# Kernel optimization log

Measured on AMD Instinct MI355X. Metric: run time of the kernel, lower is better.

## Reference

```python
import jax, jax.numpy as jnp
import numpy as np

GROUP = 16   # self.group
K = 3        # self.k (top-3 motif rows)


def _unfold3(x):
    # nn.Unfold(kernel_size=3): [B,C,H,W] -> [B, C*9, (H-2)*(W-2)]
    # torch channel ordering: c-major, then kernel offsets row-major.
    B, C, H, W = x.shape
    Ho, Wo = H - 2, W - 2
    pats = jnp.stack([x[:, :, i:i + Ho, j:j + Wo]
                      for i in range(3) for j in range(3)], axis=2)  # [B,C,9,Ho,Wo]
    return pats.reshape(B, C * 9, Ho * Wo)


def _fold3(y, H, W):
    # nn.Fold(output_size=(H,W), kernel_size=3): sum overlapping patches back.
    B, C9, L = y.shape
    C = C9 // 9
    Ho, Wo = H - 2, W - 2
    y = y.reshape(B, C, 3, 3, Ho, Wo)
    out = jnp.zeros((B, C, H, W), y.dtype)
    for i in range(3):
        for j in range(3):
            out = out.at[:, :, i:i + Ho, j:j + Wo].add(y[:, :, i, j])
    return out


def _group_motif(xg, H, W):
    motif = _unfold3(xg)                                  # [B,P,L], P = Cg*9
    B, P, L = motif.shape
    # torch.cdist (p=2) between the P rows, via the Gram trick.
    sq = jnp.sum(motif * motif, axis=-1)                  # [B,P]
    gram = jnp.einsum('bpl,bql->bpq', motif, motif)       # [B,P,P]
    d2 = sq[:, :, None] + sq[:, None, :] - 2.0 * gram
    dist = jnp.sqrt(jnp.maximum(d2, 0.0))
    eye = jnp.eye(P, dtype=bool)[None]
    dist = jnp.where(eye, jnp.inf, dist)                  # diagonal := inf
    # topk(k=1, largest=False) == argmin over last dim
    min_idx = jnp.argmin(dist, axis=-1)                   # [B,P] int
    # torch.unique(return_counts=True) over the whole tensor (flattened over batch)
    counts = jnp.bincount(min_idx.ravel(), length=P)      # [P] int
    # sort counts descending, take first K uniques -> lax.top_k
    top_c, top_i = jax.lax.top_k(counts, K)               # [K],[K]
    total = jnp.sum(top_c).astype(motif.dtype)
    rows = motif[:, top_i, :]                             # [B,K,L] gathered motif rows
    cf = top_c.astype(motif.dtype)
    motif_new = jnp.zeros_like(motif)
    for o in range(K):
        # torch: motif * motif[:, u_o].unsqueeze(1) * c_o // total  (floor division)
        motif_new = motif_new + jnp.floor(motif * rows[:, o][:, None, :] * cf[o] / total)
    return _fold3(motif_new, H, W)


def setup_inputs() -> dict:
    key = jax.random.key(0)
    feature = jax.random.normal(key, (2, 256, 192, 192), dtype=jnp.float32)
    return {"feature": feature}


def reference(feature):
    B, C, H, W = feature.shape
    chunks = jnp.split(feature, GROUP, axis=1)
    outs = [_group_motif(g, H, W) for g in chunks]
    return jnp.concatenate(outs, axis=1)                  # [B, C, H, W]
```

## Files before the change

### kernel.cpp

```cpp
#include <hip/hip_runtime.h>
#include <math.h>

#define NB 2
#define NC 256
#define CG 16
#define HH 192
#define WW 192
#define HO 190
#define PP 144

typedef float v2f __attribute__((ext_vector_type(2)));

#define SMEM_FLOATS 5684

#define GLD16(GP, LP)                                                         \
    __builtin_amdgcn_global_load_lds(                                         \
        (const __attribute__((address_space(1))) void*)(GP),                  \
        (__attribute__((address_space(3))) void*)(LP), 16, 0, 0)

__global__ __launch_bounds__(192, 2) void gram_kernel(const float* __restrict__ x,
                                                      double* __restrict__ gram)
{
    __shared__ __align__(16) float smem[SMEM_FLOATS];
    float* const red2 = smem + 2548;
    float* const ebuf = smem + 4948;

    const int v = threadIdx.x;
    const int p = v & 1;
    const int bb = (v + 2) & ~1;

    const int bid = blockIdx.x;
    const int vx = bid & 7;
    const int tq = bid >> 3;
    const int idxw = tq / 36;
    const int rr0 = tq - idxw * 36;
    const int hg = idxw * 8 + vx;
    const int bg = hg >> 1;
    int r = rr0 + 36 * (hg & 1);
    int c2 = 0;
    while (r >= (c2 + 2) / 2) { r -= (c2 + 2) / 2; ++c2; }
    const int c1a = 2 * r;
    int c1b = 2 * r + 1;
    const bool bval = (c1b <= c2);
    if (!bval) c1b = c2;
    const int b = bg >> 4, g = bg & 15;

    const float* __restrict__ xa  = x + ((size_t)(b * NC + g * CG + c1a)) * (HH * WW);
    const float* __restrict__ xb  = x + ((size_t)(b * NC + g * CG + c1b)) * (HH * WW);
    const float* __restrict__ x2g = x + ((size_t)(b * NC + g * CG + c2 )) * (HH * WW);

    v2f midA[15], midB[15];
#pragma unroll
    for (int o = 0; o < 15; ++o) { midA[o] = (v2f){0.f, 0.f}; midB[o] = (v2f){0.f, 0.f}; }

    v2f win[6][3];
    float ca[6], cb[6];
#pragma unroll
    for (int k = 0; k < 6; ++k) {
        ca[k] = xa[(size_t)(2 + k) * WW + v];
        cb[k] = xb[(size_t)(2 + k) * WW + v];
    }

    const float* pa = xa + (size_t)8 * WW + v;
    const float* pb = xb + (size_t)8 * WW + v;
    int lds_off;

#define USTEP6(P, WPF, GPF)                                                   \
    {                                                                         \
        const float a1 = ca[(P)];                                             \
        const float b1 = cb[(P)];                                             \
        if (GPF) { ca[(P)] = pa[(P) * WW]; cb[(P)] = pb[(P) * WW]; }          \
        if (WPF) {                                                            \
            _Pragma("unroll")                                                 \
            for (int pr = 0; pr < 3; ++pr)                                    \
                win[((P) + 5) % 6][pr] = *(const v2f*)(&smem[lds_off + 2 * pr]); \
        }                                                                     \
        lds_off += 196;                                                       \
        const v2f a2 = (v2f){a1, a1};                                         \
        const v2f b2 = (v2f){b1, b1};                                         \
        _Pragma("unroll")                                                     \
        for (int kk = 0; kk < 5; ++kk) {                                      \
            _Pragma("unroll")                                                 \
            for (int pr = 0; pr < 3; ++pr) {                                  \
                const v2f wv = win[((P) + kk) % 6][pr];                       \
                midA[kk * 3 + pr] = __builtin_elementwise_fma(a2, wv, midA[kk * 3 + pr]); \
                midB[kk * 3 + pr] = __builtin_elementwise_fma(b2, wv, midB[kk * 3 + pr]); \
            }                                                                 \
        }                                                                     \
    }

#define STAGE(ROW0, NROUND, LASTN)                                            \
    __syncthreads();                                                          \
    _Pragma("unroll")                                                         \
    for (int rr2 = 0; rr2 < (NROUND); ++rr2) {                                \
        if (rr2 < (NROUND) - 1 || v < (LASTN)) {                              \
            const int slot = rr2 * 192 + v;                                   \
            const int row = slot / 49;                                        \
            const int s49 = slot - row * 49;                                  \
            const int col = (s49 == 0) ? 0 : (s49 - 1) * 4;                   \
            const float* gp2 = x2g + (size_t)((ROW0) + row) * WW + col;       \
            float* lp = smem + (rr2 * 192 + (v & ~63)) * 4;                   \
            GLD16(gp2, lp);                                                   \
        }                                                                     \
    }                                                                         \
    __syncthreads();                                                          \
    if (v < 116) smem[(v >> 2) * 196 + (v & 3)] = 0.f;                        \
    __syncthreads();

    for (int band = 0; band < 7; ++band) {
        STAGE(band * 24, 8, 77)

        if (band == 0) {
#pragma unroll
            for (int k = 0; k < 5; ++k)
#pragma unroll
            for (int pr = 0; pr < 3; ++pr)
                win[k][pr] = *(const v2f*)(&smem[k * 196 + bb + 2 * pr]);
        }

        lds_off = 5 * 196 + bb;
        for (int it = 0; it < 4; ++it) {
            USTEP6(0, 1, 1) USTEP6(1, 1, 1) USTEP6(2, 1, 1)
            USTEP6(3, 1, 1) USTEP6(4, 1, 1) USTEP6(5, 1, 1)
            pa += 6 * WW; pb += 6 * WW;
        }
    }
    STAGE(168, 7, 24)
    lds_off = 5 * 196 + bb;
    USTEP6(0, 1, 1) USTEP6(1, 1, 1) USTEP6(2, 1, 1)
    USTEP6(3, 1, 1) USTEP6(4, 1, 1) USTEP6(5, 1, 1)
    pa += 6 * WW; pb += 6 * WW;
    USTEP6(0, 1, 1) USTEP6(1, 1, 1) USTEP6(2, 1, 1)
    USTEP6(3, 1, 1) USTEP6(4, 1, 1) USTEP6(5, 1, 1)
    pa += 6 * WW; pb += 6 * WW;
    USTEP6(0, 1, 1) USTEP6(1, 1, 1) USTEP6(2, 1, 0)
    USTEP6(3, 1, 0) USTEP6(4, 1, 0) USTEP6(5, 1, 0)
    USTEP6(0, 1, 0) USTEP6(1, 0, 0)
#undef USTEP6
#undef STAGE

    __syncthreads();
    for (int i = 0; i < 12; ++i) {
        const int ar = (i < 6) ? (i - 2) : (188 + i - 6);
        const float val = (ar >= 0 && ar <= 191) ? x2g[(size_t)ar * WW + v] : 0.f;
        smem[i * 196 + 4 + v] = val;
    }
    __syncthreads();

    double* const gp = gram + (size_t)bg * (PP * PP);

#define EPI_CW(KQ, DJ, CVAL)                                                  \
    ({                                                                        \
        float ve_, vo_;                                                       \
        { const int pr_ = (DJ) >> 1, ln_ = (DJ) & 1;                          \
          const v2f m_ = ((CVAL) == 0) ? midA[(KQ) * 3 + pr_] : midB[(KQ) * 3 + pr_]; \
          ve_ = ln_ ? m_.y : m_.x; }                                          \
        { const int pr_ = ((DJ) + 1) >> 1, ln_ = ((DJ) + 1) & 1;              \
          const v2f m_ = ((CVAL) == 0) ? midA[(KQ) * 3 + pr_] : midB[(KQ) * 3 + pr_]; \
          vo_ = ln_ ? m_.y : m_.x; }                                          \
        float cw_ = p ? vo_ : ve_;                                            \
        cw_ = fmaf(xra, smem[bufa * 196 + 2 + v + (DJ)], cw_);                \
        cw_ = fmaf(xrb, smem[bufb * 196 + 2 + v + (DJ)], cw_);                \
        cw_;                                                                  \
    })

#pragma unroll
    for (int i1 = 0; i1 < 3; ++i1) {
        const int ra = (i1 == 0) ? 0 : ((i1 == 1) ? 1 : 190);
        const int rb = (i1 == 0) ? 1 : ((i1 == 1) ? 190 : 191);
#pragma unroll
        for (int c = 0; c < 2; ++c) {
            const float* __restrict__ xc = (c == 0) ? xa : xb;
            const float xra = xc[(size_t)ra * WW + v];
            const float xrb = xc[(size_t)rb * WW + v];
            if (v >= 96) {
#pragma unroll
                for (int k = 0; k < 5; ++k) {
                    const int bufa = (ra < 2) ? (ra + k) : (ra + k - 184);
                    const int bufb = (rb < 2) ? (rb + k) : (rb + k - 184);
#pragma unroll
                    for (int dj = 0; dj < 5; ++dj)
                        red2[(v - 96) * 25 + k * 5 + dj] = EPI_CW(k, dj, c);
                }
            } else if (v < 2) {
#pragma unroll
                for (int k = 0; k < 5; ++k) {
                    const int bufa = (ra < 2) ? (ra + k) : (ra + k - 184);
                    const int bufb = (rb < 2) ? (rb + k) : (rb + k - 184);
#pragma unroll
                    for (int dj = 0; dj < 5; ++dj)
                        ebuf[v * 25 + k * 5 + dj] = EPI_CW(k, dj, c);
                }
            }
            __syncthreads();
            float e0 = 0.f, e1 = 0.f, e190 = 0.f, e191 = 0.f;
            if (v < 25) {
                e0   = ebuf[v];
                e1   = ebuf[25 + v];
                e190 = red2[94 * 25 + v];
                e191 = red2[95 * 25 + v];
            }
            __syncthreads();
            if (v < 96) {
#pragma unroll
                for (int k = 0; k < 5; ++k) {
                    const int bufa = (ra < 2) ? (ra + k) : (ra + k - 184);
                    const int bufb = (rb < 2) ? (rb + k) : (rb + k - 184);
#pragma unroll
                    for (int dj = 0; dj < 5; ++dj)
                        red2[v * 25 + k * 5 + dj] += EPI_CW(k, dj, c);
                }
            }
            __syncthreads();
#pragma unroll
            for (int s = 48; s >= 3; s >>= 1) {
                for (int idx = v; idx < s * 25; idx += 192) {
                    const int vv = idx / 25, o = idx - vv * 25;
                    red2[vv * 25 + o] += red2[(vv + s) * 25 + o];
                }
                __syncthreads();
            }
            if (v < 25 && (c == 0 || bval)) {
                const int di = v / 5 - 2, dj = v - (v / 5) * 5 - 2;
                const int i2 = i1 + di;
                if (i2 >= 0 && i2 <= 2) {
                    const float S = red2[0 * 25 + v] + red2[1 * 25 + v] + red2[2 * 25 + v];
                    const int c1 = (c == 0) ? c1a : c1b;
#pragma unroll
                    for (int j1 = 0; j1 < 3; ++j1) {
                        const int j2 = j1 + dj;
                        if (j2 < 0 || j2 > 2) continue;
                        const float W = S - ((j1 == 0) ? (e190 + e191)
                                          : (j1 == 1) ? (e0 + e191)
                                                      : (e0 + e1));
                        const int pp = c1 * 9 + i1 * 3 + j1;
                        const int qq = c2 * 9 + i2 * 3 + j2;
                        gp[pp * PP + qq] = (double)W;
                        if (c1 != c2) gp[qq * PP + pp] = (double)W;
                    }
                }
            }
            __syncthreads();
        }
    }
#undef EPI_CW
}

__global__ __launch_bounds__(320) void topk_kernel(const double* __restrict__ gram,
                                                   float* __restrict__ pf,
                                                   int* __restrict__ pi)
{
    const int g = blockIdx.x;
    __shared__ double sdiag[2][PP];
    __shared__ int counts[PP];
    const int tid = threadIdx.x;
    if (tid < PP) counts[tid] = 0;
    if (tid < 2 * PP) {
        const int b = tid / PP, p = tid % PP;
        const double* gb = gram + (size_t)(b * 16 + g) * (PP * PP);
        sdiag[b][p] = gb[p * PP + p];
    }
    __syncthreads();
    if (tid < 2 * PP) {
        const int b = tid / PP, p = tid % PP;
        const double* row = gram + ((size_t)(b * 16 + g) * PP + p) * PP;
        const double sp = sdiag[b][p];
        double best = 1e300;
        int bi = 0;
        for (int q = 0; q < PP; ++q) {
            if (q == p) continue;
            const double d2 = sp + sdiag[b][q] - 2.0 * row[q];
            if (d2 < best) { best = d2; bi = q; }
        }
        atomicAdd(&counts[bi], 1);
    }
    __syncthreads();
    if (tid == 0) {
        int sel[3], cv[3];
        for (int o = 0; o < 3; ++o) {
            int bc = -1, bp = 0;
            for (int p = 0; p < PP; ++p) {
                bool taken = false;
                for (int u = 0; u < o; ++u) if (sel[u] == p) taken = true;
                if (!taken && counts[p] > bc) { bc = counts[p]; bp = p; }
            }
            sel[o] = bp; cv[o] = bc;
        }
        const int tot = cv[0] + cv[1] + cv[2];
        for (int o = 0; o < 3; ++o) {
            pf[g * 4 + o] = (float)cv[o];
            pi[g * 4 + o] = sel[o];
        }
        pf[g * 4 + 3] = (float)tot;
    }
}

template <bool EDGE>
__device__ __forceinline__ void motif_quad(const float* __restrict__ x,
                                           const float* __restrict__ pf,
                                           const int* __restrict__ pi,
                                           float* __restrict__ out,
                                           int b, int ch, int h, int w0)
{
    const int g = ch >> 4;
    const size_t base = ((size_t)(b * NC + ch)) * (HH * WW);
    const float4 xv4 = *(const float4*)(x + base + (size_t)h * WW + w0);
    const float xs[4] = {xv4.x, xv4.y, xv4.z, xv4.w};
    float acc[4] = {0.f, 0.f, 0.f, 0.f};
    const float total = pf[g * 4 + 3];
    const float rcp = (float)(1.0 / (double)total);

#pragma unroll
    for (int o = 0; o < 3; ++o) {
        const int p = pi[g * 4 + o];
        const float cff = pf[g * 4 + o];
        const int co = p / 9;
        const int kk = p - co * 9;
        const int io = kk / 3, jo = kk - (kk / 3) * 3;
        const float* Rb = x + ((size_t)(b * NC + g * CG + co)) * (HH * WW);
#pragma unroll
        for (int i = 0; i < 3; ++i) {
            const int ho = h - i;
            bool rowok = true;
            int hr = ho + io;
            if (EDGE) {
                rowok = (ho >= 0) && (ho < HO);
                hr = hr < 0 ? 0 : (hr > HH - 1 ? HH - 1 : hr);
            }
            const float* row = Rb + (size_t)hr * WW;
            float rv[6];
#pragma unroll
            for (int u = 0; u < 6; ++u) {
                int col = w0 - 2 + jo + u;
                if (EDGE) col = col < 0 ? 0 : (col > WW - 1 ? WW - 1 : col);
                rv[u] = row[col];
            }
#pragma unroll
            for (int j = 0; j < 3; ++j)
#pragma unroll
            for (int q = 0; q < 4; ++q) {
                const float r2 = rv[q - j + 2];
                const float t1 = xs[q] * r2;
                const float t2 = t1 * cff;
                const float q0 = t2 * rcp;
                const float rr = fmaf(-total, q0, t2);
                const float qf = fmaf(rr, rcp, q0);
                const float vfl = floorf(qf);
                if (EDGE) {
                    const int wo = w0 + q - j;
                    const bool ok = rowok && (wo >= 0) && (wo < HO);
                    acc[q] += ok ? vfl : 0.f;
                } else {
                    acc[q] += vfl;
                }
            }
        }
    }
    float4 ov = make_float4(acc[0], acc[1], acc[2], acc[3]);
    *(float4*)(out + base + (size_t)h * WW + w0) = ov;
}

#define NBLK_INT 17296
#define NBLK_EDGE 1136

__global__ __launch_bounds__(256) void out_kernel(const float* __restrict__ x,
                                                  const float* __restrict__ pf,
                                                  const int* __restrict__ pi,
                                                  float* __restrict__ out)
{
    const int bid = blockIdx.x;
    if (bid < NBLK_INT) {
        const int gid = bid * 256 + threadIdx.x;
        const int w4i = gid % 46;
        int t = gid / 46;
        const int h = 2 + t % 188; t /= 188;
        const int ch = t & 255;
        const int b = t >> 8;
        motif_quad<false>(x, pf, pi, out, b, ch, h, (w4i + 1) * 4);
    } else {
        const int gid = (bid - NBLK_INT) * 256 + threadIdx.x;
        const int e = gid % 568;
        int t = gid / 568;
        const int ch = t & 255;
        const int b = t >> 8;
        int h, w4;
        if (e < 192) {
            const int hs = e / 48;
            h = (hs < 2) ? hs : 188 + hs;
            w4 = e % 48;
        } else {
            const int e2 = e - 192;
            h = 2 + (e2 >> 1);
            w4 = (e2 & 1) ? 47 : 0;
        }
        motif_quad<true>(x, pf, pi, out, b, ch, h, w4 * 4);
    }
}

extern "C" void kernel_launch(void* const* d_in, const int* in_sizes, int n_in,
                              void* d_out, int out_size, void* d_ws, size_t ws_size,
                              hipStream_t stream)
{
    const float* x = (const float*)d_in[0];
    float* out = (float*)d_out;

    double* gram = (double*)d_ws;
    const size_t gram_bytes = (size_t)32 * PP * PP * sizeof(double);
    float* pf = (float*)((char*)d_ws + gram_bytes);
    int* pi = (int*)((char*)d_ws + gram_bytes + 256);

    gram_kernel<<<2304, 192, 0, stream>>>(x, gram);
    topk_kernel<<<16, 320, 0, stream>>>(gram, pf, pi);
    out_kernel<<<NBLK_INT + NBLK_EDGE, 256, 0, stream>>>(x, pf, pi, out);
}
```

Measured before the change: 351.2 us.

## Merge two-channel epilogue reduction, hoist LDS pad zeroing, pack interior motif math

The gram kernel epilogue now reduces both channel columns (c1a and c1b) in a single pass, using a 51-float stride, which halves the number of barrier-separated reduction rounds. The zeroing of the LDS pad columns moves out of every band stage to one write before the loop, and pad-column global loads are skipped, which removes one barrier per band. The interior output kernel uses packed v2f multiplies and FMAs for the floor-division math. The trade-off is more LDS per block, which can reduce occupancy, and extra register pressure in the epilogue.

```diff
diff --git a/kernel.cpp b/kernel.cpp
--- a/kernel.cpp
+++ b/kernel.cpp
@@ -11,7 +11,7 @@
 
 typedef float v2f __attribute__((ext_vector_type(2)));
 
-#define SMEM_FLOATS 5684
+#define SMEM_FLOATS 7544
 
 #define GLD16(GP, LP)                                                         \
     __builtin_amdgcn_global_load_lds(                                         \
@@ -23,7 +23,7 @@
 {
     __shared__ __align__(16) float smem[SMEM_FLOATS];
     float* const red2 = smem + 2548;
-    float* const ebuf = smem + 4948;
+    float* const ebuf = smem + 7444;
 
     const int v = threadIdx.x;
     const int p = v & 1;
@@ -48,6 +48,9 @@
     const float* __restrict__ xa  = x + ((size_t)(b * NC + g * CG + c1a)) * (HH * WW);
     const float* __restrict__ xb  = x + ((size_t)(b * NC + g * CG + c1b)) * (HH * WW);
     const float* __restrict__ x2g = x + ((size_t)(b * NC + g * CG + c2 )) * (HH * WW);
+
+    if (v < 116) smem[(v >> 2) * 196 + (v & 3)] = 0.f;
+    else if (v < 118) smem[5568 + v] = 0.f;
 
     v2f midA[15], midB[15];
 #pragma unroll
@@ -97,14 +100,13 @@
             const int slot = rr2 * 192 + v;                                   \
             const int row = slot / 49;                                        \
             const int s49 = slot - row * 49;                                  \
-            const int col = (s49 == 0) ? 0 : (s49 - 1) * 4;                   \
-            const float* gp2 = x2g + (size_t)((ROW0) + row) * WW + col;       \
-            float* lp = smem + (rr2 * 192 + (v & ~63)) * 4;                   \
-            GLD16(gp2, lp);                                                   \
+            if (s49 != 0) {                                                   \
+                const float* gp2 = x2g + (size_t)((ROW0) + row) * WW + (s49 - 1) * 4; \
+                float* lp = smem + (rr2 * 192 + (v & ~63)) * 4;               \
+                GLD16(gp2, lp);                                               \
+            }                                                                 \
         }                                                                     \
     }                                                                         \
-    __syncthreads();                                                          \
-    if (v < 116) smem[(v >> 2) * 196 + (v & 3)] = 0.f;                        \
     __syncthreads();
 
     for (int band = 0; band < 7; ++band) {
@@ -149,7 +151,7 @@
 
     double* const gp = gram + (size_t)bg * (PP * PP);
 
-#define EPI_CW(KQ, DJ, CVAL)                                                  \
+#define EPI_CW(KQ, DJ, CVAL, XRA, XRB)                                        \
     ({                                                                        \
         float ve_, vo_;                                                       \
         { const int pr_ = (DJ) >> 1, ln_ = (DJ) & 1;                          \
@@ -159,8 +161,8 @@
           const v2f m_ = ((CVAL) == 0) ? midA[(KQ) * 3 + pr_] : midB[(KQ) * 3 + pr_]; \
           vo_ = ln_ ? m_.y : m_.x; }                                          \
         float cw_ = p ? vo_ : ve_;                                            \
-        cw_ = fmaf(xra, smem[bufa * 196 + 2 + v + (DJ)], cw_);                \
-        cw_ = fmaf(xrb, smem[bufb * 196 + 2 + v + (DJ)], cw_);                \
+        cw_ = fmaf((XRA), smem[bufa * 196 + 2 + v + (DJ)], cw_);              \
+        cw_ = fmaf((XRB), smem[bufb * 196 + 2 + v + (DJ)], cw_);              \
         cw_;                                                                  \
     })
 
@@ -168,63 +170,74 @@
     for (int i1 = 0; i1 < 3; ++i1) {
         const int ra = (i1 == 0) ? 0 : ((i1 == 1) ? 1 : 190);
         const int rb = (i1 == 0) ? 1 : ((i1 == 1) ? 190 : 191);
-#pragma unroll
-        for (int c = 0; c < 2; ++c) {
-            const float* __restrict__ xc = (c == 0) ? xa : xb;
-            const float xra = xc[(size_t)ra * WW + v];
-            const float xrb = xc[(size_t)rb * WW + v];
-            if (v >= 96) {
-#pragma unroll
-                for (int k = 0; k < 5; ++k) {
-                    const int bufa = (ra < 2) ? (ra + k) : (ra + k - 184);
-                    const int bufb = (rb < 2) ? (rb + k) : (rb + k - 184);
-#pragma unroll
-                    for (int dj = 0; dj < 5; ++dj)
-                        red2[(v - 96) * 25 + k * 5 + dj] = EPI_CW(k, dj, c);
+        const float xra0 = xa[(size_t)ra * WW + v];
+        const float xrb0 = xa[(size_t)rb * WW + v];
+        const float xra1 = xb[(size_t)ra * WW + v];
+        const float xrb1 = xb[(size_t)rb * WW + v];
+        if (v >= 96) {
+            float* dst = red2 + (v - 96) * 51;
+#pragma unroll
+            for (int k = 0; k < 5; ++k) {
+                const int bufa = (ra < 2) ? (ra + k) : (ra + k - 184);
+                const int bufb = (rb < 2) ? (rb + k) : (rb + k - 184);
+#pragma unroll
+                for (int dj = 0; dj < 5; ++dj) {
+                    dst[k * 5 + dj]      = EPI_CW(k, dj, 0, xra0, xrb0);
+                    dst[25 + k * 5 + dj] = EPI_CW(k, dj, 1, xra1, xrb1);
                 }
-            } else if (v < 2) {
-#pragma unroll
-                for (int k = 0; k < 5; ++k) {
-                    const int bufa = (ra < 2) ? (ra + k) : (ra + k - 184);
-                    const int bufb = (rb < 2) ? (rb + k) : (rb + k - 184);
-#pragma unroll
-                    for (int dj = 0; dj < 5; ++dj)
-                        ebuf[v * 25 + k * 5 + dj] = EPI_CW(k, dj, c);
+            }
+        } else if (v < 2) {
+            float* dst = ebuf + v * 50;
+#pragma unroll
+            for (int k = 0; k < 5; ++k) {
+                const int bufa = (ra < 2) ? (ra + k) : (ra + k - 184);
+                const int bufb = (rb < 2) ? (rb + k) : (rb + k - 184);
+#pragma unroll
+                for (int dj = 0; dj < 5; ++dj) {
+                    dst[k * 5 + dj]      = EPI_CW(k, dj, 0, xra0, xrb0);
+                    dst[25 + k * 5 + dj] = EPI_CW(k, dj, 1, xra1, xrb1);
                 }
             }
+        }
+        __syncthreads();
+        float e0 = 0.f, e1 = 0.f, e190 = 0.f, e191 = 0.f;
+        if (v < 50) {
+            e0   = ebuf[v];
+            e1   = ebuf[50 + v];
+            e190 = red2[94 * 51 + v];
+            e191 = red2[95 * 51 + v];
+        }
+        __syncthreads();
+        if (v < 96) {
+            float* dst = red2 + v * 51;
+#pragma unroll
+            for (int k = 0; k < 5; ++k) {
+                const int bufa = (ra < 2) ? (ra + k) : (ra + k - 184);
+                const int bufb = (rb < 2) ? (rb + k) : (rb + k - 184);
+#pragma unroll
+                for (int dj = 0; dj < 5; ++dj) {
+                    dst[k * 5 + dj]      += EPI_CW(k, dj, 0, xra0, xrb0);
+                    dst[25 + k * 5 + dj] += EPI_CW(k, dj, 1, xra1, xrb1);
+                }
+            }
+        }
+        __syncthreads();
+#pragma unroll
+        for (int s = 48; s >= 3; s >>= 1) {
+            for (int idx = v; idx < s * 50; idx += 192) {
+                const int vv = idx / 50, o = idx - vv * 50;
+                red2[vv * 51 + o] += red2[(vv + s) * 51 + o];
+            }
             __syncthreads();
-            float e0 = 0.f, e1 = 0.f, e190 = 0.f, e191 = 0.f;
-            if (v < 25) {
-                e0   = ebuf[v];
-                e1   = ebuf[25 + v];
-                e190 = red2[94 * 25 + v];
-                e191 = red2[95 * 25 + v];
-            }
-            __syncthreads();
-            if (v < 96) {
-#pragma unroll
-                for (int k = 0; k < 5; ++k) {
-                    const int bufa = (ra < 2) ? (ra + k) : (ra + k - 184);
-                    const int bufb = (rb < 2) ? (rb + k) : (rb + k - 184);
-#pragma unroll
-                    for (int dj = 0; dj < 5; ++dj)
-                        red2[v * 25 + k * 5 + dj] += EPI_CW(k, dj, c);
-                }
-            }
-            __syncthreads();
-#pragma unroll
-            for (int s = 48; s >= 3; s >>= 1) {
-                for (int idx = v; idx < s * 25; idx += 192) {
-                    const int vv = idx / 25, o = idx - vv * 25;
-                    red2[vv * 25 + o] += red2[(vv + s) * 25 + o];
-                }
-                __syncthreads();
-            }
-            if (v < 25 && (c == 0 || bval)) {
-                const int di = v / 5 - 2, dj = v - (v / 5) * 5 - 2;
+        }
+        if (v < 50) {
+            const int c = v / 25;
+            const int o = v - c * 25;
+            if (c == 0 || bval) {
+                const int di = o / 5 - 2, dj = o - (o / 5) * 5 - 2;
                 const int i2 = i1 + di;
                 if (i2 >= 0 && i2 <= 2) {
-                    const float S = red2[0 * 25 + v] + red2[1 * 25 + v] + red2[2 * 25 + v];
+                    const float S = red2[0 * 51 + v] + red2[1 * 51 + v] + red2[2 * 51 + v];
                     const int c1 = (c == 0) ? c1a : c1b;
 #pragma unroll
                     for (int j1 = 0; j1 < 3; ++j1) {
@@ -240,8 +253,8 @@
                     }
                 }
             }
-            __syncthreads();
-        }
+        }
+        __syncthreads();
     }
 #undef EPI_CW
 }
@@ -295,12 +308,69 @@
     }
 }
 
-template <bool EDGE>
-__device__ __forceinline__ void motif_quad(const float* __restrict__ x,
-                                           const float* __restrict__ pf,
-                                           const int* __restrict__ pi,
-                                           float* __restrict__ out,
-                                           int b, int ch, int h, int w0)
+__device__ __forceinline__ void motif_quad_pk(const float* __restrict__ x,
+                                              const float* __restrict__ pf,
+                                              const int* __restrict__ pi,
+                                              float* __restrict__ out,
+                                              int b, int ch, int h, int w0)
+{
+    const int g = ch >> 4;
+    const size_t base = ((size_t)(b * NC + ch)) * (HH * WW);
+    const float4 xv4 = *(const float4*)(x + base + (size_t)h * WW + w0);
+    const v2f xp01 = (v2f){xv4.x, xv4.y};
+    const v2f xp23 = (v2f){xv4.z, xv4.w};
+    v2f acc01 = (v2f){0.f, 0.f}, acc23 = (v2f){0.f, 0.f};
+    const float total = pf[g * 4 + 3];
+    const float rcp = (float)(1.0 / (double)total);
+    const v2f rcp2 = (v2f){rcp, rcp};
+    const v2f ntot2 = (v2f){-total, -total};
+
+#pragma unroll
+    for (int o = 0; o < 3; ++o) {
+        const int p = pi[g * 4 + o];
+        const float cff = pf[g * 4 + o];
+        const v2f cf2 = (v2f){cff, cff};
+        const int co = p / 9;
+        const int kk = p - co * 9;
+        const int io = kk / 3, jo = kk - (kk / 3) * 3;
+        const float* Rb = x + ((size_t)(b * NC + g * CG + co)) * (HH * WW);
+#pragma unroll
+        for (int i = 0; i < 3; ++i) {
+            const float* row = Rb + (size_t)(h - i + io) * WW;
+            float rv[6];
+#pragma unroll
+            for (int u = 0; u < 6; ++u)
+                rv[u] = row[w0 - 2 + jo + u];
+#pragma unroll
+            for (int j = 0; j < 3; ++j) {
+                const v2f r01 = (v2f){rv[2 - j], rv[3 - j]};
+                const v2f r23 = (v2f){rv[4 - j], rv[5 - j]};
+                const v2f t1a = xp01 * r01;
+                const v2f t1b = xp23 * r23;
+                const v2f t2a = t1a * cf2;
+                const v2f t2b = t1b * cf2;
+                const v2f q0a = t2a * rcp2;
+                const v2f q0b = t2b * rcp2;
+                const v2f rra = __builtin_elementwise_fma(ntot2, q0a, t2a);
+                const v2f rrb = __builtin_elementwise_fma(ntot2, q0b, t2b);
+                const v2f qfa = __builtin_elementwise_fma(rra, rcp2, q0a);
+                const v2f qfb = __builtin_elementwise_fma(rrb, rcp2, q0b);
+                acc01.x += floorf(qfa.x);
+                acc01.y += floorf(qfa.y);
+                acc23.x += floorf(qfb.x);
+                acc23.y += floorf(qfb.y);
+            }
+        }
+    }
+    float4 ov = make_float4(acc01.x, acc01.y, acc23.x, acc23.y);
+    *(float4*)(out + base + (size_t)h * WW + w0) = ov;
+}
+
+__device__ __forceinline__ void motif_quad_edge(const float* __restrict__ x,
+                                                const float* __restrict__ pf,
+                                                const int* __restrict__ pi,
+                                                float* __restrict__ out,
+                                                int b, int ch, int h, int w0)
 {
     const int g = ch >> 4;
     const size_t base = ((size_t)(b * NC + ch)) * (HH * WW);
@@ -321,18 +391,15 @@
 #pragma unroll
         for (int i = 0; i < 3; ++i) {
             const int ho = h - i;
-            bool rowok = true;
+            const bool rowok = (ho >= 0) && (ho < HO);
             int hr = ho + io;
-            if (EDGE) {
-                rowok = (ho >= 0) && (ho < HO);
-                hr = hr < 0 ? 0 : (hr > HH - 1 ? HH - 1 : hr);
-            }
+            hr = hr < 0 ? 0 : (hr > HH - 1 ? HH - 1 : hr);
             const float* row = Rb + (size_t)hr * WW;
             float rv[6];
 #pragma unroll
             for (int u = 0; u < 6; ++u) {
                 int col = w0 - 2 + jo + u;
-                if (EDGE) col = col < 0 ? 0 : (col > WW - 1 ? WW - 1 : col);
+                col = col < 0 ? 0 : (col > WW - 1 ? WW - 1 : col);
                 rv[u] = row[col];
             }
 #pragma unroll
@@ -346,13 +413,9 @@
                 const float rr = fmaf(-total, q0, t2);
                 const float qf = fmaf(rr, rcp, q0);
                 const float vfl = floorf(qf);
-                if (EDGE) {
-                    const int wo = w0 + q - j;
-                    const bool ok = rowok && (wo >= 0) && (wo < HO);
-                    acc[q] += ok ? vfl : 0.f;
-                } else {
-                    acc[q] += vfl;
-                }
+                const int wo = w0 + q - j;
+                const bool ok = rowok && (wo >= 0) && (wo < HO);
+                acc[q] += ok ? vfl : 0.f;
             }
         }
     }
@@ -376,7 +439,7 @@
         const int h = 2 + t % 188; t /= 188;
         const int ch = t & 255;
         const int b = t >> 8;
-        motif_quad<false>(x, pf, pi, out, b, ch, h, (w4i + 1) * 4);
+        motif_quad_pk(x, pf, pi, out, b, ch, h, (w4i + 1) * 4);
     } else {
         const int gid = (bid - NBLK_INT) * 256 + threadIdx.x;
         const int e = gid % 568;
@@ -393,7 +456,7 @@
             h = 2 + (e2 >> 1);
             w4 = (e2 & 1) ? 47 : 0;
         }
-        motif_quad<true>(x, pf, pi, out, b, ch, h, w4 * 4);
+        motif_quad_edge(x, pf, pi, out, b, ch, h, w4 * 4);
     }
 }
 
```

After: 346.8 us. No clear change (-1.3%).
